# Kernel tuning notes

Hardware: AMD Instinct MI355X
Metric: run time of the kernel (lower is better)

Reference implementation:

```python
import jax, jax.numpy as jnp
import numpy as np

B, CIN, COUT, K, LDIM, HW = 16, 512, 512, 3, 512, 32


def setup_inputs() -> dict:
    key = jax.random.key(0)
    ks = jax.random.split(key, 4)
    return {
        "x": jax.random.normal(ks[0], (B, CIN, HW, HW), jnp.float32),
        "w": jax.random.normal(ks[1], (B, LDIM), jnp.float32),
        "mod_w": jax.random.normal(ks[2], (CIN, LDIM), jnp.float32) * 0.02,
        "mod_b": jnp.zeros((CIN,), jnp.float32),
        "ln_g": jnp.ones((CIN,), jnp.float32),
        "ln_b": jnp.zeros((CIN,), jnp.float32),
        "weight": jax.random.normal(ks[3], (COUT, CIN, K, K), jnp.float32) * 0.02,
        "scale": jnp.ones((1, CIN, 1, 1), jnp.float32),
    }


def reference(x, w, mod_w, mod_b, ln_g, ln_b, weight, scale):
    eps = 1e-8
    b, cin, H, W = x.shape
    cout, _, k, _ = weight.shape
    # modulation MLP: Linear -> LayerNorm -> LeakyReLU(0.2)
    s = w @ mod_w.T + mod_b                                   # [b, cin]
    mu = s.mean(-1, keepdims=True)
    var = s.var(-1, keepdims=True)
    s = (s - mu) * jax.lax.rsqrt(var + 1e-5) * ln_g + ln_b
    s = jnp.where(s >= 0, s, 0.2 * s)
    # modulate per-sample weights: [b, cout, cin, k, k]
    s = s.reshape(b, 1, cin, 1, 1) * scale.reshape(1, 1, cin, 1, 1)
    wmod = weight[None] * s
    # demodulate
    d = jax.lax.rsqrt(jnp.sum(wmod * wmod, axis=(2, 3, 4)) + eps)  # [b, cout]
    wmod = wmod * d.reshape(b, cout, 1, 1, 1)
    # batch-as-groups conv2d
    wg = wmod.reshape(b * cout, cin, k, k)
    xg = x.reshape(1, b * cin, H, W)
    pad = k // 2
    out = jax.lax.conv_general_dilated(
        xg, wg, window_strides=(1, 1), padding=[(pad, pad), (pad, pad)],
        dimension_numbers=("NCHW", "OIHW", "NCHW"), feature_group_count=b)
    return out.reshape(b, cout, H, W)
```

## Files before the change

kernel.cpp:

```cpp
#include <hip/hip_runtime.h>

typedef unsigned short u16;
typedef __bf16 bf16x8 __attribute__((ext_vector_type(8)));
typedef float  f32x16 __attribute__((ext_vector_type(16)));

__device__ __forceinline__ u16 f2bf(float f) {
    union { float f; unsigned u; } v; v.f = f;
    return (u16)((v.u + 0x7fffu + ((v.u >> 16) & 1u)) >> 16);
}

#define GLD16(gsrc, ldst) \
    __builtin_amdgcn_global_load_lds( \
        (const __attribute__((address_space(1))) void*)(gsrc), \
        (__attribute__((address_space(3))) void*)(ldst), 16, 0, 0)

__global__ __launch_bounds__(256) void lin_kernel(
    const float* __restrict__ w, const float* __restrict__ mod_w,
    const float* __restrict__ mod_b, float* __restrict__ s_raw)
{
    int gw = (blockIdx.x * 256 + threadIdx.x) >> 6;
    int lane = threadIdx.x & 63;
    int b = gw >> 9, c = gw & 511;
    const float* wr = w + b * 512;
    const float* mr = mod_w + (size_t)c * 512;
    float a = 0.f;
#pragma unroll
    for (int i = 0; i < 8; ++i)
        a = fmaf(wr[lane + i * 64], mr[lane + i * 64], a);
    for (int off = 32; off; off >>= 1) a += __shfl_down(a, off);
    if (!lane) s_raw[gw] = a + mod_b[c];
}

__global__ __launch_bounds__(512) void norm_kernel(
    const float* __restrict__ s_raw, const float* __restrict__ ln_g,
    const float* __restrict__ ln_b, const float* __restrict__ scale,
    float* __restrict__ s_eff)
{
    int b = blockIdx.x, c = threadIdx.x;
    __shared__ float rs[512], rq[512];
    float s = s_raw[b * 512 + c];
    rs[c] = s; rq[c] = s * s;
    __syncthreads();
    for (int off = 256; off; off >>= 1) {
        if (c < off) { rs[c] += rs[c + off]; rq[c] += rq[c + off]; }
        __syncthreads();
    }
    float mean = rs[0] * (1.f / 512.f);
    float var  = rq[0] * (1.f / 512.f) - mean * mean;
    float sn = (s - mean) * rsqrtf(var + 1e-5f) * ln_g[c] + ln_b[c];
    sn = sn >= 0.f ? sn : 0.2f * sn;
    s_eff[b * 512 + c] = sn * scale[c];
}

__global__ __launch_bounds__(256) void wsq_kernel(
    const float* __restrict__ weight, float* __restrict__ wsq, u16* __restrict__ wbfT)
{
    int idx = blockIdx.x * 256 + threadIdx.x;
    int co = idx >> 9, ci = idx & 511;
    int cg = ci >> 3, cj = ci & 7;
    const float* wp = weight + (size_t)idx * 9;
    float s = 0.f;
#pragma unroll
    for (int p = 0; p < 9; ++p) {
        float v = wp[p];
        s += v * v;
        wbfT[((size_t)(p * 64 + cg) * 512 + co) * 8 + cj] = f2bf(v);
    }
    wsq[idx] = s;
}

__global__ __launch_bounds__(256) void xs_kernel(
    const float* __restrict__ x, const float* __restrict__ s_eff,
    u16* __restrict__ xs)
{
    const int bh = blockIdx.x;
    const int b = bh >> 5, h = bh & 31;
    __shared__ float tile[64][33];
    for (int c0 = 0; c0 < 512; c0 += 64) {
        if (c0) __syncthreads();
        for (int idx = threadIdx.x; idx < 2048; idx += 256) {
            int c = idx >> 5, ww = idx & 31;
            tile[c][ww] = x[(((size_t)b * 512 + c0 + c) * 32 + h) * 32 + ww]
                          * s_eff[b * 512 + c0 + c];
        }
        __syncthreads();
        for (int idx = threadIdx.x; idx < 2048; idx += 256) {
            int ww = idx >> 6, c = idx & 63;
            xs[((b * 32 + h) * 32 + ww) * 512 + c0 + c] = f2bf(tile[c][ww]);
        }
    }
}

__global__ __launch_bounds__(256) void dsc_kernel(
    const float* __restrict__ s_eff, const float* __restrict__ wsq,
    float* __restrict__ dsc)
{
    int gw = (blockIdx.x * 256 + threadIdx.x) >> 6;
    int lane = threadIdx.x & 63;
    int b = gw >> 9, co = gw & 511;
    float a = 0.f;
#pragma unroll
    for (int i = 0; i < 8; ++i) {
        int cin = lane + i * 64;
        float se = s_eff[b * 512 + cin];
        a += se * se * wsq[co * 512 + cin];
    }
    for (int off = 32; off; off >>= 1) a += __shfl_down(a, off);
    if (!lane) dsc[gw] = rsqrtf(a + 1e-8f);
}

__global__ void zfill_kernel(float* p) { p[threadIdx.x] = 0.f; }

__global__ __launch_bounds__(256, 2) void conv_kernel(
    const u16* __restrict__ wbfT,
    const u16* __restrict__ xs,
    const float* __restrict__ dsc,
    const u16* __restrict__ zp,
    float* __restrict__ out)
{
    __shared__ __align__(16) u16 lds[2 * 544 * 8];

    const int tid  = threadIdx.x;
    const int lane = tid & 63;
    const int wv   = tid >> 6;
    const int l31  = lane & 31;
    const int kc8  = lane >> 5;

    const int bx = blockIdx.x;
    const int mt = bx & 1;
    const int nt = bx >> 1;
    const int b  = nt >> 4;
    const int h0 = (nt & 15) << 1;

    const u16* xsb = xs + (size_t)b * (32 * 32 * 512);

    const u16* sb[3]; bool sval[3], inb[3];
#pragma unroll
    for (int k = 0; k < 3; ++k) {
        int ch = tid + k * 256;
        sval[k] = ch < 544;
        int p = ch >> 2, slot = ch & 3;
        int kc = slot ^ ((p >> 1) & 3);
        int rr = p / 34, cc = p % 34;
        int hh = h0 - 1 + rr, ww = cc - 1;
        inb[k] = sval[k] && ((unsigned)hh < 32u) && ((unsigned)ww < 32u);
        sb[k] = xsb + (hh * 32 + ww) * 512 + kc * 8;
    }
    char* ldsb = (char*)lds;
    char* wdst = ldsb + wv * 1024;

    auto stage = [&](int buf, int c0) {
        char* d = wdst + buf * 8704;
        GLD16(inb[0] ? sb[0] + c0 : zp, d);
        GLD16(inb[1] ? sb[1] + c0 : zp, d + 4096);
        if (sval[2]) GLD16(inb[2] ? sb[2] + c0 : zp, d + 8192);
    };

    const u16* apb[2];
#pragma unroll
    for (int mf = 0; mf < 2; ++mf)
        apb[mf] = wbfT + ((size_t)kc8 * 512 + mt * 256 + wv * 64 + mf * 32 + l31) * 8;

    uint4 aA[2][2], aB[2][2];
    auto loadA = [&](uint4 (&dst)[2][2], int pos, int c0g) {
#pragma unroll
        for (int mf = 0; mf < 2; ++mf)
#pragma unroll
            for (int kk = 0; kk < 2; ++kk)
                dst[mf][kk] = *reinterpret_cast<const uint4*>(
                    apb[mf] + ((size_t)(pos * 64 + c0g) + kk * 2) * 4096);
    };

    bf16x8 bvA[2][2], bvB[2][2];
    auto loadB = [&](bf16x8 (&dst)[2][2], const char* base, int pos) {
        const int kh = pos / 3, kw = pos % 3;
#pragma unroll
        for (int kk = 0; kk < 2; ++kk) {
            const int sk = kk * 2 + kc8;
#pragma unroll
            for (int nf = 0; nf < 2; ++nf) {
                const int p = (nf + kh) * 34 + l31 + kw;
                dst[kk][nf] = *reinterpret_cast<const bf16x8*>(
                    base + p * 64 + ((sk ^ ((p >> 1) & 3)) << 4));
            }
        }
    };

    f32x16 acc[2][2] = {};
    auto domfma = [&](uint4 (&af)[2][2], bf16x8 (&bf)[2][2]) {
#pragma unroll
        for (int kk = 0; kk < 2; ++kk)
#pragma unroll
            for (int mf = 0; mf < 2; ++mf) {
                bf16x8 av = *reinterpret_cast<const bf16x8*>(&af[mf][kk]);
                acc[mf][0] = __builtin_amdgcn_mfma_f32_32x32x16_bf16(
                    av, bf[kk][0], acc[mf][0], 0, 0, 0);
                acc[mf][1] = __builtin_amdgcn_mfma_f32_32x32x16_bf16(
                    av, bf[kk][1], acc[mf][1], 0, 0, 0);
            }
    };

    stage(0, 0);
    loadA(aA, 0, 0);
    __syncthreads();

    for (int r = 0; r < 16; ++r) {
        const int c0g = r * 4;
        const char* base = ldsb + (r & 1) * 8704;
        if (r < 15) stage((r + 1) & 1, (r + 1) * 32);
        loadB(bvA, base, 0);

#pragma unroll
        for (int pos = 0; pos < 9; ++pos) {
            if (pos < 8) {
                if ((pos & 1) == 0) { loadA(aB, pos + 1, c0g); loadB(bvB, base, pos + 1); }
                else                { loadA(aA, pos + 1, c0g); loadB(bvA, base, pos + 1); }
            } else if (r < 15) {
                loadA(aB, 0, c0g + 4);
            }
            if ((pos & 1) == 0) domfma(aA, bvA);
            else                domfma(aB, bvB);
        }
        if (r < 15) {
#pragma unroll
            for (int mf = 0; mf < 2; ++mf)
#pragma unroll
                for (int kk = 0; kk < 2; ++kk) aA[mf][kk] = aB[mf][kk];
            asm volatile("s_waitcnt vmcnt(4)" ::: "memory");
            __builtin_amdgcn_s_barrier();
            asm volatile("" ::: "memory");
        }
    }

    const float* db = dsc + b * 512;
#pragma unroll
    for (int mf = 0; mf < 2; ++mf) {
#pragma unroll
        for (int nf = 0; nf < 2; ++nf) {
            const int h = h0 + nf, w = l31;
#pragma unroll
            for (int q = 0; q < 16; ++q) {
                int row = (q & 3) + 8 * (q >> 2) + 4 * kc8;
                int co  = mt * 256 + wv * 64 + mf * 32 + row;
                out[(((size_t)b * 512 + co) * 32 + h) * 32 + w]
                    = acc[mf][nf][q] * db[co];
            }
        }
    }
}

extern "C" void kernel_launch(void* const* d_in, const int* in_sizes, int n_in,
                              void* d_out, int out_size, void* d_ws, size_t ws_size,
                              hipStream_t stream) {
    const float* x      = (const float*)d_in[0];
    const float* w      = (const float*)d_in[1];
    const float* mod_w  = (const float*)d_in[2];
    const float* mod_b  = (const float*)d_in[3];
    const float* ln_g   = (const float*)d_in[4];
    const float* ln_b   = (const float*)d_in[5];
    const float* weight = (const float*)d_in[6];
    const float* scale  = (const float*)d_in[7];
    float* out = (float*)d_out;

    char* ws = (char*)d_ws;
    float* s_raw = (float*)(ws);
    float* dsc   = (float*)(ws);
    float* s_eff = (float*)(ws + 32768);
    float* wsq   = (float*)(ws + 65536);
    u16*   wbfT  = (u16*)(ws + 65536 + 1048576);
    u16*   xs    = (u16*)(ws + 65536 + 1048576 + 4718592);
    if (ws_size < 22609920u) return;

    lin_kernel <<<2048, 256, 0, stream>>>(w, mod_w, mod_b, s_raw);
    wsq_kernel <<<1024, 256, 0, stream>>>(weight, wsq, wbfT);
    norm_kernel<<<16, 512, 0, stream>>>(s_raw, ln_g, ln_b, scale, s_eff);
    xs_kernel  <<<512, 256, 0, stream>>>(x, s_eff, xs);
    dsc_kernel <<<2048, 256, 0, stream>>>(s_eff, wsq, dsc);
    zfill_kernel<<<1, 1024, 0, stream>>>(s_eff);
    conv_kernel<<<512, 256, 0, stream>>>(wbfT, xs, dsc, (const u16*)s_eff, out);
}
```

Baseline: 135.7 us.

## Halve conv output tile to one row per block and double grid

Each conv block now computes a single output row instead of two. That halves the LDS input halo, the per-wave accumulators and B-fragment registers, and doubles the grid to 1024 blocks. Launch bounds are raised to allow four blocks per CU for more occupancy and latency hiding. MFMA sections are wrapped with s_setprio to favour the matrix work. The trade-off is that each weight (A) fragment loaded from global memory is reused across half as many output pixels, which roughly doubles weight traffic per output.

```diff
diff --git a/kernel.cpp b/kernel.cpp
--- a/kernel.cpp
+++ b/kernel.cpp
@@ -111,14 +111,14 @@
 
 __global__ void zfill_kernel(float* p) { p[threadIdx.x] = 0.f; }
 
-__global__ __launch_bounds__(256, 2) void conv_kernel(
+__global__ __launch_bounds__(256, 4) void conv_kernel(
     const u16* __restrict__ wbfT,
     const u16* __restrict__ xs,
     const float* __restrict__ dsc,
     const u16* __restrict__ zp,
     float* __restrict__ out)
 {
-    __shared__ __align__(16) u16 lds[2 * 544 * 8];
+    __shared__ __align__(16) u16 lds[2 * 408 * 8];
 
     const int tid  = threadIdx.x;
     const int lane = tid & 63;
@@ -129,16 +129,16 @@
     const int bx = blockIdx.x;
     const int mt = bx & 1;
     const int nt = bx >> 1;
-    const int b  = nt >> 4;
-    const int h0 = (nt & 15) << 1;
+    const int b  = nt >> 5;
+    const int h0 = nt & 31;
 
     const u16* xsb = xs + (size_t)b * (32 * 32 * 512);
 
-    const u16* sb[3]; bool sval[3], inb[3];
-#pragma unroll
-    for (int k = 0; k < 3; ++k) {
+    const u16* sb[2]; bool sval[2], inb[2];
+#pragma unroll
+    for (int k = 0; k < 2; ++k) {
         int ch = tid + k * 256;
-        sval[k] = ch < 544;
+        sval[k] = ch < 408;
         int p = ch >> 2, slot = ch & 3;
         int kc = slot ^ ((p >> 1) & 3);
         int rr = p / 34, cc = p % 34;
@@ -147,13 +147,11 @@
         sb[k] = xsb + (hh * 32 + ww) * 512 + kc * 8;
     }
     char* ldsb = (char*)lds;
-    char* wdst = ldsb + wv * 1024;
 
     auto stage = [&](int buf, int c0) {
-        char* d = wdst + buf * 8704;
+        char* d = ldsb + buf * 6528 + wv * 1024;
         GLD16(inb[0] ? sb[0] + c0 : zp, d);
-        GLD16(inb[1] ? sb[1] + c0 : zp, d + 4096);
-        if (sval[2]) GLD16(inb[2] ? sb[2] + c0 : zp, d + 8192);
+        if (sval[1]) GLD16(inb[1] ? sb[1] + c0 : zp, d + 4096);
     };
 
     const u16* apb[2];
@@ -171,33 +169,30 @@
                     apb[mf] + ((size_t)(pos * 64 + c0g) + kk * 2) * 4096);
     };
 
-    bf16x8 bvA[2][2], bvB[2][2];
-    auto loadB = [&](bf16x8 (&dst)[2][2], const char* base, int pos) {
+    bf16x8 bvA[2], bvB[2];
+    auto loadB = [&](bf16x8 (&dst)[2], const char* base, int pos) {
         const int kh = pos / 3, kw = pos % 3;
+        const int p = kh * 34 + l31 + kw;
 #pragma unroll
         for (int kk = 0; kk < 2; ++kk) {
             const int sk = kk * 2 + kc8;
-#pragma unroll
-            for (int nf = 0; nf < 2; ++nf) {
-                const int p = (nf + kh) * 34 + l31 + kw;
-                dst[kk][nf] = *reinterpret_cast<const bf16x8*>(
-                    base + p * 64 + ((sk ^ ((p >> 1) & 3)) << 4));
-            }
-        }
-    };
-
-    f32x16 acc[2][2] = {};
-    auto domfma = [&](uint4 (&af)[2][2], bf16x8 (&bf)[2][2]) {
+            dst[kk] = *reinterpret_cast<const bf16x8*>(
+                base + p * 64 + ((sk ^ ((p >> 1) & 3)) << 4));
+        }
+    };
+
+    f32x16 acc[2] = {};
+    auto domfma = [&](uint4 (&af)[2][2], bf16x8 (&bf)[2]) {
+        __builtin_amdgcn_s_setprio(1);
 #pragma unroll
         for (int kk = 0; kk < 2; ++kk)
 #pragma unroll
             for (int mf = 0; mf < 2; ++mf) {
                 bf16x8 av = *reinterpret_cast<const bf16x8*>(&af[mf][kk]);
-                acc[mf][0] = __builtin_amdgcn_mfma_f32_32x32x16_bf16(
-                    av, bf[kk][0], acc[mf][0], 0, 0, 0);
-                acc[mf][1] = __builtin_amdgcn_mfma_f32_32x32x16_bf16(
-                    av, bf[kk][1], acc[mf][1], 0, 0, 0);
+                acc[mf] = __builtin_amdgcn_mfma_f32_32x32x16_bf16(
+                    av, bf[kk], acc[mf], 0, 0, 0);
             }
+        __builtin_amdgcn_s_setprio(0);
     };
 
     stage(0, 0);
@@ -206,7 +201,7 @@
 
     for (int r = 0; r < 16; ++r) {
         const int c0g = r * 4;
-        const char* base = ldsb + (r & 1) * 8704;
+        const char* base = ldsb + (r & 1) * 6528;
         if (r < 15) stage((r + 1) & 1, (r + 1) * 32);
         loadB(bvA, base, 0);
 
@@ -236,15 +231,11 @@
 #pragma unroll
     for (int mf = 0; mf < 2; ++mf) {
 #pragma unroll
-        for (int nf = 0; nf < 2; ++nf) {
-            const int h = h0 + nf, w = l31;
-#pragma unroll
-            for (int q = 0; q < 16; ++q) {
-                int row = (q & 3) + 8 * (q >> 2) + 4 * kc8;
-                int co  = mt * 256 + wv * 64 + mf * 32 + row;
-                out[(((size_t)b * 512 + co) * 32 + h) * 32 + w]
-                    = acc[mf][nf][q] * db[co];
-            }
+        for (int q = 0; q < 16; ++q) {
+            int row = (q & 3) + 8 * (q >> 2) + 4 * kc8;
+            int co  = mt * 256 + wv * 64 + mf * 32 + row;
+            out[(((size_t)b * 512 + co) * 32 + h0) * 32 + l31]
+                = acc[mf][q] * db[co];
         }
     }
 }
@@ -277,5 +268,5 @@
     xs_kernel  <<<512, 256, 0, stream>>>(x, s_eff, xs);
     dsc_kernel <<<2048, 256, 0, stream>>>(s_eff, wsq, dsc);
     zfill_kernel<<<1, 1024, 0, stream>>>(s_eff);
-    conv_kernel<<<512, 256, 0, stream>>>(wbfT, xs, dsc, (const u16*)s_eff, out);
-}
+    conv_kernel<<<1024, 256, 0, stream>>>(wbfT, xs, dsc, (const u16*)s_eff, out);
+}
```

After: 146.1 us. +7.7%, slower.
